# Kernel optimization log

Hardware: AMD Instinct MI355X
Metric: run time of the kernel (lower is better)

The kernel has to match this reference:

```python
import jax, jax.numpy as jnp
import numpy as np

# Dims: N=batch graphs, V=grid nodes (128x128), D=feature dim, E=edges, L=gnn layers
N, V, D, E, L = 16, 16384, 128, 65536, 2
EPS = 1e-5  # BatchNorm1d default eps


def setup_inputs() -> dict:
    key = jax.random.key(0)
    ks = jax.random.split(key, 8)
    H = jax.random.normal(ks[0], (N, V, D), dtype=jnp.float32)
    edge_src = jax.random.randint(ks[1], (E,), 0, V, dtype=jnp.int32)
    edge_dst = jax.random.randint(ks[2], (E,), 0, V, dtype=jnp.int32)
    A_vals = jax.random.uniform(ks[3], (E,), dtype=jnp.float32)
    scale = 1.0 / np.sqrt(D).astype(np.float32)
    # Stacked per-layer params. Linear stores weight as [out, in]; y = x @ W.T
    W_self = jax.random.normal(ks[4], (L, D, D), dtype=jnp.float32) * scale
    W_nei = jax.random.normal(ks[5], (L, D, D), dtype=jnp.float32) * scale
    gamma = jnp.ones((L, D), dtype=jnp.float32)
    beta = jnp.zeros((L, D), dtype=jnp.float32)
    return {"H": H, "edge_src": edge_src, "edge_dst": edge_dst, "A_vals": A_vals,
            "W_self": W_self, "W_nei": W_nei, "gamma": gamma, "beta": beta}


def reference(H, edge_src, edge_dst, A_vals, W_self, W_nei, gamma, beta):
    X = H  # [N, V, D]
    for l in range(L):
        # SpMM: X_nei[n] = A_norm @ X[n], batched over N via vmap.
        msg = X[:, edge_src, :] * A_vals[None, :, None]  # [N, E, D]
        X_nei = jax.vmap(
            lambda m: jax.ops.segment_sum(m, edge_dst, num_segments=V)
        )(msg)  # [N, V, D]
        # y = x @ W.T for torch Linear(weight=[out,in])
        Y = (jnp.einsum('nvd,ed->nve', X, W_self[l])
             + jnp.einsum('nvd,ed->nve', X_nei, W_nei[l]))  # [N, V, D]
        # BatchNorm1d in training mode over the flattened (N*V) batch dim
        mean = jnp.mean(Y, axis=(0, 1))            # [D]
        var = jnp.var(Y, axis=(0, 1))              # biased variance, [D]
        Y = (Y - mean) * jax.lax.rsqrt(var + EPS) * gamma[l] + beta[l]
        X = jax.nn.relu(Y)
    return X
```

## Files before the change

kernel.cpp:

```cpp
#include <hip/hip_runtime.h>

#define N_ 16
#define V_ 16384
#define D_ 128
#define E_ 65536
#define L_ 2
#define M_ (N_*V_)


typedef __attribute__((ext_vector_type(8))) short short8;
typedef __attribute__((ext_vector_type(4))) float floatx4;

__device__ inline unsigned short f2bf(float x){
  unsigned u = __builtin_bit_cast(unsigned, x);
  unsigned r = u + 0x7fffu + ((u >> 16) & 1u);
  return (unsigned short)(r >> 16);
}
__device__ inline float bf2f(unsigned short h){
  unsigned u = ((unsigned)h) << 16;
  return __builtin_bit_cast(float, u);
}
__device__ inline unsigned pack2(float a, float b){
  return (unsigned)f2bf(a) | ((unsigned)f2bf(b) << 16);
}

__global__ __launch_bounds__(256) void conv_in_k(const float* __restrict__ H,
                                                 unsigned short* __restrict__ Xb){
  int v = blockIdx.x;
  int t = threadIdx.x;
  int n = t >> 4, dc = t & 15;
  const float4* h4 = (const float4*)H;
  size_t base = ((size_t)n * V_ + v) * 32 + (size_t)dc * 2;
  float4 a = h4[base], b = h4[base + 1];
  uint4 o;
  o.x = pack2(a.x, a.y);
  o.y = pack2(a.z, a.w);
  o.z = pack2(b.x, b.y);
  o.w = pack2(b.z, b.w);
  ((uint4*)Xb)[(size_t)v * 256 + t] = o;
}

__global__ __launch_bounds__(256) void conv_w_k(const float* __restrict__ Wself,
                                                const float* __restrict__ Wnei,
                                                unsigned short* __restrict__ Wb){
  int f = blockIdx.x * 256 + threadIdx.x;
  int lane = f & 63;
  int ct   = (f >> 6) & 7;
  int ks   = (f >> 9) & 3;
  int mat  = (f >> 11) & 1;
  int l    = (f >> 12) & 1;
  int e = ct * 16 + (lane & 15);
  int d = ks * 32 + (lane >> 4) * 8;
  const float* src = (mat ? Wnei : Wself) + ((size_t)l * D_ * D_ + e * D_ + d);
  uint4 o;
  o.x = pack2(src[0], src[1]);
  o.y = pack2(src[2], src[3]);
  o.z = pack2(src[4], src[5]);
  o.w = pack2(src[6], src[7]);
  ((uint4*)Wb)[f] = o;
}

__global__ __launch_bounds__(256) void hist_k(const int* __restrict__ dst, int* __restrict__ cnt){
  int e = blockIdx.x * 256 + threadIdx.x;
  atomicAdd(&cnt[dst[e]], 1);
}

__global__ __launch_bounds__(256) void scan_k(const int* __restrict__ cnt, int* __restrict__ row_ptr){
  __shared__ int part[256];
  int t = threadIdx.x;
  int base = t * 64;
  int s = 0;
  for (int i = 0; i < 64; ++i) s += cnt[base + i];
  part[t] = s;
  __syncthreads();
  for (int d = 1; d < 256; d <<= 1){
    int v = (t >= d) ? part[t - d] : 0;
    __syncthreads();
    part[t] += v;
    __syncthreads();
  }
  int off = part[t] - s;
  for (int i = 0; i < 64; ++i){
    row_ptr[base + i] = off;
    off += cnt[base + i];
  }
  if (t == 255) row_ptr[V_] = off;
}

__global__ __launch_bounds__(256) void scatter_k(const int* __restrict__ src,
                                                 const int* __restrict__ dst,
                                                 const float* __restrict__ vals,
                                                 const int* __restrict__ row_ptr,
                                                 int* __restrict__ fill,
                                                 int* __restrict__ csr_col,
                                                 float* __restrict__ csr_val){
  int e = blockIdx.x * 256 + threadIdx.x;
  int d = dst[e];
  int pos = row_ptr[d] + atomicAdd(&fill[d], 1);
  csr_col[pos] = src[e];
  csr_val[pos] = vals[e];
}

__global__ __launch_bounds__(256, 2) void gemm_k(const unsigned short* __restrict__ X,
                                                 const uint4* __restrict__ Wfrag,
                                                 const int* __restrict__ row_ptr,
                                                 const int* __restrict__ csr_col,
                                                 const float* __restrict__ csr_val,
                                                 unsigned short* __restrict__ Yb,
                                                 float* __restrict__ stats){
  __shared__ uint4 lds_w[4096];
  __shared__ float lds_red[4 * 256];
  int tid = threadIdx.x;
  for (int i = tid; i < 4096; i += 256) lds_w[i] = Wfrag[i];

  int wave = tid >> 6, lane = tid & 63;
  int quad = lane >> 4, l15 = lane & 15;
  int row0 = blockIdx.x * 128 + wave * 32;
  int v0 = row0 >> 4;

  short8 a_s[2][4];
#pragma unroll
  for (int rt = 0; rt < 2; ++rt)
#pragma unroll
    for (int ks = 0; ks < 4; ++ks)
      a_s[rt][ks] = *(const short8*)(X + (size_t)(row0 + rt * 16 + l15) * 128 + ks * 32 + quad * 8);

  int r0a = row_ptr[v0], r1a = row_ptr[v0 + 1], r1b = row_ptr[v0 + 2];

  float accn[2][4][8];
#pragma unroll
  for (int rt = 0; rt < 2; ++rt)
#pragma unroll
    for (int ks = 0; ks < 4; ++ks)
#pragma unroll
      for (int j = 0; j < 8; ++j) accn[rt][ks][j] = 0.f;

#pragma unroll
  for (int rt = 0; rt < 2; ++rt){
    int r0 = rt ? r1a : r0a;
    int r1 = rt ? r1b : r1a;
    if (r0 < r1){
      int c = csr_col[r0];
      float a = csr_val[r0];
      for (int i = r0; i < r1; ++i){
        int ip = (i + 1 < r1) ? i + 1 : i;
        int cn = csr_col[ip];
        float an = csr_val[ip];
        const unsigned short* rp = X + ((size_t)c * 16 + l15) * 128 + quad * 8;
        short8 w0 = *(const short8*)(rp);
        short8 w1 = *(const short8*)(rp + 32);
        short8 w2 = *(const short8*)(rp + 64);
        short8 w3 = *(const short8*)(rp + 96);
#pragma unroll
        for (int j = 0; j < 8; ++j) accn[rt][0][j] += a * bf2f((unsigned short)w0[j]);
#pragma unroll
        for (int j = 0; j < 8; ++j) accn[rt][1][j] += a * bf2f((unsigned short)w1[j]);
#pragma unroll
        for (int j = 0; j < 8; ++j) accn[rt][2][j] += a * bf2f((unsigned short)w2[j]);
#pragma unroll
        for (int j = 0; j < 8; ++j) accn[rt][3][j] += a * bf2f((unsigned short)w3[j]);
        c = cn; a = an;
      }
    }
  }
  short8 a_n[2][4];
#pragma unroll
  for (int rt = 0; rt < 2; ++rt)
#pragma unroll
    for (int ks = 0; ks < 4; ++ks)
#pragma unroll
      for (int j = 0; j < 8; ++j) a_n[rt][ks][j] = (short)f2bf(accn[rt][ks][j]);

  __syncthreads();

  floatx4 zero = {0.f, 0.f, 0.f, 0.f};
  floatx4 acc[2][8];
#pragma unroll
  for (int rt = 0; rt < 2; ++rt)
#pragma unroll
    for (int ct = 0; ct < 8; ++ct) acc[rt][ct] = zero;

  const short8* lw = (const short8*)lds_w;
#pragma unroll
  for (int ks = 0; ks < 4; ++ks){
#pragma unroll
    for (int ct = 0; ct < 8; ++ct){
      short8 bs = lw[((0 * 4 + ks) * 8 + ct) * 64 + lane];
      short8 bn = lw[((1 * 4 + ks) * 8 + ct) * 64 + lane];
#pragma unroll
      for (int rt = 0; rt < 2; ++rt){
        acc[rt][ct] = __builtin_amdgcn_mfma_f32_16x16x32_bf16(a_s[rt][ks], bs, acc[rt][ct], 0, 0, 0);
        acc[rt][ct] = __builtin_amdgcn_mfma_f32_16x16x32_bf16(a_n[rt][ks], bn, acc[rt][ct], 0, 0, 0);
      }
    }
  }

  float* wred = lds_red + wave * 256;
#pragma unroll
  for (int rt = 0; rt < 2; ++rt){
    int rowq = row0 + rt * 16 + quad * 4;
#pragma unroll
    for (int ct = 0; ct < 8; ++ct){
      int col = ct * 16 + l15;
      float s = 0.f, q = 0.f;
#pragma unroll
      for (int rg = 0; rg < 4; ++rg){
        float yv = acc[rt][ct][rg];
        Yb[(size_t)(rowq + rg) * 128 + col] = f2bf(yv);
        s += yv; q += yv * yv;
      }
      s += __shfl_xor(s, 16); s += __shfl_xor(s, 32);
      q += __shfl_xor(q, 16); q += __shfl_xor(q, 32);
      if (lane < 16){
        if (rt == 0) wred[ct * 16 + lane] = s; else wred[ct * 16 + lane] += s;
      } else if (lane < 32){
        int c2 = ct * 16 + (lane & 15);
        if (rt == 0) wred[128 + c2] = q; else wred[128 + c2] += q;
      }
    }
  }
  __syncthreads();
  {
    float tot = lds_red[tid] + lds_red[256 + tid] + lds_red[512 + tid] + lds_red[768 + tid];
    int col = tid & 127;
    int slot = blockIdx.x & 63;
    float* dstp = (tid < 128) ? (stats + slot * 128 + col)
                              : (stats + 64 * 128 + slot * 128 + col);
    atomicAdd(dstp, tot);
  }
}

__global__ __launch_bounds__(128) void finalize_k(const float* __restrict__ stats,
                                                  const float* __restrict__ gamma,
                                                  const float* __restrict__ beta,
                                                  float* __restrict__ scsh){
  int d = threadIdx.x;
  float s0=0.f,s1=0.f,s2=0.f,s3=0.f,q0=0.f,q1=0.f,q2=0.f,q3=0.f;
  for (int k = 0; k < 64; k += 4){
    s0 += stats[(k+0) * 128 + d];
    s1 += stats[(k+1) * 128 + d];
    s2 += stats[(k+2) * 128 + d];
    s3 += stats[(k+3) * 128 + d];
    q0 += stats[64*128 + (k+0) * 128 + d];
    q1 += stats[64*128 + (k+1) * 128 + d];
    q2 += stats[64*128 + (k+2) * 128 + d];
    q3 += stats[64*128 + (k+3) * 128 + d];
  }
  float s = (s0+s1)+(s2+s3);
  float q = (q0+q1)+(q2+q3);
  float inv = 1.0f / (float)M_;
  float mean = s * inv;
  float var  = q * inv - mean * mean;
  float rstd = rsqrtf(var + 1e-5f);
  float scale = gamma[d] * rstd;
  scsh[d]       = scale;
  scsh[128 + d] = beta[d] - mean * scale;
}

__global__ __launch_bounds__(256) void bn_mid_k(const uint4* __restrict__ Y,
                                                const float* __restrict__ scsh,
                                                uint4* __restrict__ Xo){
  int i = blockIdx.x * 256 + threadIdx.x;
  int c = (i * 8) & 127;
  uint4 y = Y[i];
  float4 sc0 = *(const float4*)(scsh + c);
  float4 sc1 = *(const float4*)(scsh + c + 4);
  float4 sh0 = *(const float4*)(scsh + 128 + c);
  float4 sh1 = *(const float4*)(scsh + 132 + c);
  float x0 = fmaxf(0.f, bf2f((unsigned short)(y.x & 0xffff)) * sc0.x + sh0.x);
  float x1 = fmaxf(0.f, bf2f((unsigned short)(y.x >> 16))    * sc0.y + sh0.y);
  float x2 = fmaxf(0.f, bf2f((unsigned short)(y.y & 0xffff)) * sc0.z + sh0.z);
  float x3 = fmaxf(0.f, bf2f((unsigned short)(y.y >> 16))    * sc0.w + sh0.w);
  float x4 = fmaxf(0.f, bf2f((unsigned short)(y.z & 0xffff)) * sc1.x + sh1.x);
  float x5 = fmaxf(0.f, bf2f((unsigned short)(y.z >> 16))    * sc1.y + sh1.y);
  float x6 = fmaxf(0.f, bf2f((unsigned short)(y.w & 0xffff)) * sc1.z + sh1.z);
  float x7 = fmaxf(0.f, bf2f((unsigned short)(y.w >> 16))    * sc1.w + sh1.w);
  uint4 o;
  o.x = pack2(x0, x1);
  o.y = pack2(x2, x3);
  o.z = pack2(x4, x5);
  o.w = pack2(x6, x7);
  Xo[i] = o;
}

__global__ __launch_bounds__(256) void bn_out_k(const uint4* __restrict__ Y,
                                                const float* __restrict__ scsh,
                                                float4* __restrict__ out){
  int v = blockIdx.x;
  int t = threadIdx.x;
  int n = t >> 4, dc = t & 15;
  uint4 y = Y[(size_t)v * 256 + t];
  int d0 = dc * 8;
  float4 sc0 = *(const float4*)(scsh + d0);
  float4 sc1 = *(const float4*)(scsh + d0 + 4);
  float4 sh0 = *(const float4*)(scsh + 128 + d0);
  float4 sh1 = *(const float4*)(scsh + 128 + d0 + 4);
  float4 o0, o1;
  o0.x = fmaxf(0.f, bf2f((unsigned short)(y.x & 0xffff)) * sc0.x + sh0.x);
  o0.y = fmaxf(0.f, bf2f((unsigned short)(y.x >> 16))    * sc0.y + sh0.y);
  o0.z = fmaxf(0.f, bf2f((unsigned short)(y.y & 0xffff)) * sc0.z + sh0.z);
  o0.w = fmaxf(0.f, bf2f((unsigned short)(y.y >> 16))    * sc0.w + sh0.w);
  o1.x = fmaxf(0.f, bf2f((unsigned short)(y.z & 0xffff)) * sc1.x + sh1.x);
  o1.y = fmaxf(0.f, bf2f((unsigned short)(y.z >> 16))    * sc1.y + sh1.y);
  o1.z = fmaxf(0.f, bf2f((unsigned short)(y.w & 0xffff)) * sc1.z + sh1.z);
  o1.w = fmaxf(0.f, bf2f((unsigned short)(y.w >> 16))    * sc1.w + sh1.w);
  size_t ob = ((size_t)n * V_ + v) * 32 + (size_t)dc * 2;
  out[ob]     = o0;
  out[ob + 1] = o1;
}

static inline size_t align_up(size_t x, size_t a){ return (x + a - 1) & ~(a - 1); }

extern "C" void kernel_launch(void* const* d_in, const int* in_sizes, int n_in,
                              void* d_out, int out_size, void* d_ws, size_t ws_size,
                              hipStream_t stream){
  const float* H     = (const float*)d_in[0];
  const int*   esrc  = (const int*)  d_in[1];
  const int*   edst  = (const int*)  d_in[2];
  const float* avals = (const float*)d_in[3];
  const float* Wself = (const float*)d_in[4];
  const float* Wnei  = (const float*)d_in[5];
  const float* gamma = (const float*)d_in[6];
  const float* beta  = (const float*)d_in[7];

  char* ws = (char*)d_ws;
  size_t off = 0;
  unsigned short* Xb   = (unsigned short*)(ws + off); off += align_up((size_t)M_ * D_ * 2, 256);
  unsigned short* Y0   = (unsigned short*)(ws + off); off += align_up((size_t)M_ * D_ * 2, 256);
  unsigned short* X1   = (unsigned short*)(ws + off); off += align_up((size_t)M_ * D_ * 2, 256);
  unsigned short* Wb   = (unsigned short*)(ws + off); off += align_up((size_t)L_ * 2 * D_ * D_ * 2, 256);
  int*   row_ptr = (int*)  (ws + off); off += align_up((size_t)(V_ + 1) * 4, 256);
  int*   csr_col = (int*)  (ws + off); off += align_up((size_t)E_ * 4, 256);
  float* csr_val = (float*)(ws + off); off += align_up((size_t)E_ * 4, 256);
  float* scsh0   = (float*)(ws + off); off += align_up((size_t)2 * 128 * 4, 256);
  float* scsh1   = (float*)(ws + off); off += align_up((size_t)2 * 128 * 4, 256);
  char* zbase = ws + off;
  int*   cnt    = (int*)  (ws + off); off += (size_t)V_ * 4;
  int*   fill   = (int*)  (ws + off); off += (size_t)V_ * 4;
  float* stats0 = (float*)(ws + off); off += (size_t)64 * 128 * 2 * 4;
  float* stats1 = (float*)(ws + off); off += (size_t)64 * 128 * 2 * 4;
  size_t zbytes = (size_t)(ws + off - zbase);
  unsigned short* Y1 = Xb;
  (void)ws_size; (void)in_sizes; (void)n_in; (void)out_size;

  conv_in_k<<<V_, 256, 0, stream>>>(H, Xb);
  conv_w_k<<<8192 / 256, 256, 0, stream>>>(Wself, Wnei, Wb);
  hipMemsetAsync(zbase, 0, zbytes, stream);
  hist_k<<<E_ / 256, 256, 0, stream>>>(edst, cnt);
  scan_k<<<1, 256, 0, stream>>>(cnt, row_ptr);
  scatter_k<<<E_ / 256, 256, 0, stream>>>(esrc, edst, avals, row_ptr, fill, csr_col, csr_val);

  gemm_k<<<M_ / 128, 256, 0, stream>>>(Xb, (const uint4*)Wb,
                                       row_ptr, csr_col, csr_val, Y0, stats0);
  finalize_k<<<1, 128, 0, stream>>>(stats0, gamma, beta, scsh0);

  bn_mid_k<<<M_ * D_ / 8 / 256, 256, 0, stream>>>((const uint4*)Y0, scsh0, (uint4*)X1);

  gemm_k<<<M_ / 128, 256, 0, stream>>>(X1, (const uint4*)Wb + 4096,
                                       row_ptr, csr_col, csr_val, Y1, stats1);
  finalize_k<<<1, 128, 0, stream>>>(stats1, gamma + 128, beta + 128, scsh1);
  bn_out_k<<<V_, 256, 0, stream>>>((const uint4*)Y1, scsh1, (float4*)d_out);
}
```

Measured before the change: 500.2 us.

## Give each wave one node and prefetch neighbor rows in fused SpMM-GEMM

The fused SpMM+GEMM kernel now gives each wave one graph node (16 rows) instead of two, and each block has 8 waves (512 threads) instead of 4. The launch bound changes from (256,2) to (512,4) so more waves can be resident. The gather loop now software-pipelines the neighbor row loads by fetching the next neighbor's four vectors before accumulating the current one, to hide global-memory latency. The cost is that the LDS weight tile is shared by more waves per block while each wave does less MFMA work, and the tighter register budget could cause spills.

```diff
diff --git a/kernel.cpp b/kernel.cpp
--- a/kernel.cpp
+++ b/kernel.cpp
@@ -101,7 +101,7 @@
   csr_val[pos] = vals[e];
 }
 
-__global__ __launch_bounds__(256, 2) void gemm_k(const unsigned short* __restrict__ X,
+__global__ __launch_bounds__(512, 4) void gemm_k(const unsigned short* __restrict__ X,
                                                  const uint4* __restrict__ Wfrag,
                                                  const int* __restrict__ row_ptr,
                                                  const int* __restrict__ csr_col,
@@ -109,76 +109,69 @@
                                                  unsigned short* __restrict__ Yb,
                                                  float* __restrict__ stats){
   __shared__ uint4 lds_w[4096];
-  __shared__ float lds_red[4 * 256];
+  __shared__ float lds_red[8 * 256];
   int tid = threadIdx.x;
-  for (int i = tid; i < 4096; i += 256) lds_w[i] = Wfrag[i];
+  for (int i = tid; i < 4096; i += 512) lds_w[i] = Wfrag[i];
 
   int wave = tid >> 6, lane = tid & 63;
   int quad = lane >> 4, l15 = lane & 15;
-  int row0 = blockIdx.x * 128 + wave * 32;
-  int v0 = row0 >> 4;
-
-  short8 a_s[2][4];
-#pragma unroll
-  for (int rt = 0; rt < 2; ++rt)
-#pragma unroll
-    for (int ks = 0; ks < 4; ++ks)
-      a_s[rt][ks] = *(const short8*)(X + (size_t)(row0 + rt * 16 + l15) * 128 + ks * 32 + quad * 8);
-
-  int r0a = row_ptr[v0], r1a = row_ptr[v0 + 1], r1b = row_ptr[v0 + 2];
-
-  float accn[2][4][8];
-#pragma unroll
-  for (int rt = 0; rt < 2; ++rt)
-#pragma unroll
-    for (int ks = 0; ks < 4; ++ks)
-#pragma unroll
-      for (int j = 0; j < 8; ++j) accn[rt][ks][j] = 0.f;
-
-#pragma unroll
-  for (int rt = 0; rt < 2; ++rt){
-    int r0 = rt ? r1a : r0a;
-    int r1 = rt ? r1b : r1a;
-    if (r0 < r1){
-      int c = csr_col[r0];
-      float a = csr_val[r0];
-      for (int i = r0; i < r1; ++i){
-        int ip = (i + 1 < r1) ? i + 1 : i;
-        int cn = csr_col[ip];
-        float an = csr_val[ip];
-        const unsigned short* rp = X + ((size_t)c * 16 + l15) * 128 + quad * 8;
-        short8 w0 = *(const short8*)(rp);
-        short8 w1 = *(const short8*)(rp + 32);
-        short8 w2 = *(const short8*)(rp + 64);
-        short8 w3 = *(const short8*)(rp + 96);
-#pragma unroll
-        for (int j = 0; j < 8; ++j) accn[rt][0][j] += a * bf2f((unsigned short)w0[j]);
-#pragma unroll
-        for (int j = 0; j < 8; ++j) accn[rt][1][j] += a * bf2f((unsigned short)w1[j]);
-#pragma unroll
-        for (int j = 0; j < 8; ++j) accn[rt][2][j] += a * bf2f((unsigned short)w2[j]);
-#pragma unroll
-        for (int j = 0; j < 8; ++j) accn[rt][3][j] += a * bf2f((unsigned short)w3[j]);
-        c = cn; a = an;
-      }
+  int v = blockIdx.x * 8 + wave;
+  int row0 = v * 16;
+
+  short8 a_s[4];
+#pragma unroll
+  for (int ks = 0; ks < 4; ++ks)
+    a_s[ks] = *(const short8*)(X + (size_t)(row0 + l15) * 128 + ks * 32 + quad * 8);
+
+  int r0 = row_ptr[v], r1 = row_ptr[v + 1];
+
+  float accn[4][8];
+#pragma unroll
+  for (int ks = 0; ks < 4; ++ks)
+#pragma unroll
+    for (int j = 0; j < 8; ++j) accn[ks][j] = 0.f;
+
+  if (r0 < r1){
+    int c = csr_col[r0];
+    float a = csr_val[r0];
+    const unsigned short* rp = X + ((size_t)c * 16 + l15) * 128 + quad * 8;
+    short8 w0 = *(const short8*)(rp);
+    short8 w1 = *(const short8*)(rp + 32);
+    short8 w2 = *(const short8*)(rp + 64);
+    short8 w3 = *(const short8*)(rp + 96);
+    for (int i = r0; i < r1; ++i){
+      int ip = (i + 1 < r1) ? i + 1 : i;
+      int cn = csr_col[ip];
+      float an = csr_val[ip];
+      const unsigned short* rpn = X + ((size_t)cn * 16 + l15) * 128 + quad * 8;
+      short8 n0 = *(const short8*)(rpn);
+      short8 n1 = *(const short8*)(rpn + 32);
+      short8 n2 = *(const short8*)(rpn + 64);
+      short8 n3 = *(const short8*)(rpn + 96);
+#pragma unroll
+      for (int j = 0; j < 8; ++j) accn[0][j] += a * bf2f((unsigned short)w0[j]);
+#pragma unroll
+      for (int j = 0; j < 8; ++j) accn[1][j] += a * bf2f((unsigned short)w1[j]);
+#pragma unroll
+      for (int j = 0; j < 8; ++j) accn[2][j] += a * bf2f((unsigned short)w2[j]);
+#pragma unroll
+      for (int j = 0; j < 8; ++j) accn[3][j] += a * bf2f((unsigned short)w3[j]);
+      w0 = n0; w1 = n1; w2 = n2; w3 = n3;
+      a = an;
     }
   }
-  short8 a_n[2][4];
-#pragma unroll
-  for (int rt = 0; rt < 2; ++rt)
-#pragma unroll
-    for (int ks = 0; ks < 4; ++ks)
-#pragma unroll
-      for (int j = 0; j < 8; ++j) a_n[rt][ks][j] = (short)f2bf(accn[rt][ks][j]);
+  short8 a_n[4];
+#pragma unroll
+  for (int ks = 0; ks < 4; ++ks)
+#pragma unroll
+    for (int j = 0; j < 8; ++j) a_n[ks][j] = (short)f2bf(accn[ks][j]);
 
   __syncthreads();
 
   floatx4 zero = {0.f, 0.f, 0.f, 0.f};
-  floatx4 acc[2][8];
-#pragma unroll
-  for (int rt = 0; rt < 2; ++rt)
-#pragma unroll
-    for (int ct = 0; ct < 8; ++ct) acc[rt][ct] = zero;
+  floatx4 acc[8];
+#pragma unroll
+  for (int ct = 0; ct < 8; ++ct) acc[ct] = zero;
 
   const short8* lw = (const short8*)lds_w;
 #pragma unroll
@@ -187,41 +180,33 @@
     for (int ct = 0; ct < 8; ++ct){
       short8 bs = lw[((0 * 4 + ks) * 8 + ct) * 64 + lane];
       short8 bn = lw[((1 * 4 + ks) * 8 + ct) * 64 + lane];
-#pragma unroll
-      for (int rt = 0; rt < 2; ++rt){
-        acc[rt][ct] = __builtin_amdgcn_mfma_f32_16x16x32_bf16(a_s[rt][ks], bs, acc[rt][ct], 0, 0, 0);
-        acc[rt][ct] = __builtin_amdgcn_mfma_f32_16x16x32_bf16(a_n[rt][ks], bn, acc[rt][ct], 0, 0, 0);
-      }
+      acc[ct] = __builtin_amdgcn_mfma_f32_16x16x32_bf16(a_s[ks], bs, acc[ct], 0, 0, 0);
+      acc[ct] = __builtin_amdgcn_mfma_f32_16x16x32_bf16(a_n[ks], bn, acc[ct], 0, 0, 0);
     }
   }
 
   float* wred = lds_red + wave * 256;
-#pragma unroll
-  for (int rt = 0; rt < 2; ++rt){
-    int rowq = row0 + rt * 16 + quad * 4;
-#pragma unroll
-    for (int ct = 0; ct < 8; ++ct){
-      int col = ct * 16 + l15;
-      float s = 0.f, q = 0.f;
-#pragma unroll
-      for (int rg = 0; rg < 4; ++rg){
-        float yv = acc[rt][ct][rg];
-        Yb[(size_t)(rowq + rg) * 128 + col] = f2bf(yv);
-        s += yv; q += yv * yv;
-      }
-      s += __shfl_xor(s, 16); s += __shfl_xor(s, 32);
-      q += __shfl_xor(q, 16); q += __shfl_xor(q, 32);
-      if (lane < 16){
-        if (rt == 0) wred[ct * 16 + lane] = s; else wred[ct * 16 + lane] += s;
-      } else if (lane < 32){
-        int c2 = ct * 16 + (lane & 15);
-        if (rt == 0) wred[128 + c2] = q; else wred[128 + c2] += q;
-      }
+  int rowq = row0 + quad * 4;
+#pragma unroll
+  for (int ct = 0; ct < 8; ++ct){
+    int col = ct * 16 + l15;
+    float s = 0.f, q = 0.f;
+#pragma unroll
+    for (int rg = 0; rg < 4; ++rg){
+      float yv = acc[ct][rg];
+      Yb[(size_t)(rowq + rg) * 128 + col] = f2bf(yv);
+      s += yv; q += yv * yv;
     }
+    s += __shfl_xor(s, 16); s += __shfl_xor(s, 32);
+    q += __shfl_xor(q, 16); q += __shfl_xor(q, 32);
+    if (lane < 16)      wred[ct * 16 + lane] = s;
+    else if (lane < 32) wred[128 + ct * 16 + (lane & 15)] = q;
   }
   __syncthreads();
-  {
-    float tot = lds_red[tid] + lds_red[256 + tid] + lds_red[512 + tid] + lds_red[768 + tid];
+  if (tid < 256){
+    float tot = 0.f;
+#pragma unroll
+    for (int w = 0; w < 8; ++w) tot += lds_red[w * 256 + tid];
     int col = tid & 127;
     int slot = blockIdx.x & 63;
     float* dstp = (tid < 128) ? (stats + slot * 128 + col)
@@ -350,14 +335,14 @@
   scan_k<<<1, 256, 0, stream>>>(cnt, row_ptr);
   scatter_k<<<E_ / 256, 256, 0, stream>>>(esrc, edst, avals, row_ptr, fill, csr_col, csr_val);
 
-  gemm_k<<<M_ / 128, 256, 0, stream>>>(Xb, (const uint4*)Wb,
-                                       row_ptr, csr_col, csr_val, Y0, stats0);
+  gemm_k<<<V_ / 8, 512, 0, stream>>>(Xb, (const uint4*)Wb,
+                                     row_ptr, csr_col, csr_val, Y0, stats0);
   finalize_k<<<1, 128, 0, stream>>>(stats0, gamma, beta, scsh0);
 
   bn_mid_k<<<M_ * D_ / 8 / 256, 256, 0, stream>>>((const uint4*)Y0, scsh0, (uint4*)X1);
 
-  gemm_k<<<M_ / 128, 256, 0, stream>>>(X1, (const uint4*)Wb + 4096,
-                                       row_ptr, csr_col, csr_val, Y1, stats1);
+  gemm_k<<<V_ / 8, 512, 0, stream>>>(X1, (const uint4*)Wb + 4096,
+                                     row_ptr, csr_col, csr_val, Y1, stats1);
   finalize_k<<<1, 128, 0, stream>>>(stats1, gamma + 128, beta + 128, scsh1);
   bn_out_k<<<V_, 256, 0, stream>>>((const uint4*)Y1, scsh1, (float4*)d_out);
 }
```

Measured after the change: 460.0 us. 1.09x faster.
